# Optimization experiments

Measured on AMD Instinct MI355X. Metric: run time of the kernel, lower is better.

Reference implementation:

```python
import jax, jax.numpy as jnp
import numpy as np

EMBED_DIM = 512
NUM_HEADS = 8
HEAD_DIM = EMBED_DIM // NUM_HEADS
SCALE = 1.0 / HEAD_DIM ** 0.5


def setup_inputs() -> dict:
    key = jax.random.key(0)
    ks = jax.random.split(key, 7)
    B, C, H, W = 8, EMBED_DIM, 32, 32
    x = jax.random.normal(ks[0], (B, C, H, W), dtype=jnp.float32)
    s = 1.0 / np.sqrt(EMBED_DIM)
    return {
        "x": x,
        "ln_gamma": jnp.ones((EMBED_DIM,), jnp.float32),
        "ln_beta": jnp.zeros((EMBED_DIM,), jnp.float32),
        "w_qkv": jax.random.uniform(ks[1], (EMBED_DIM, 3 * EMBED_DIM), jnp.float32, -s, s),
        "b_qkv": jax.random.uniform(ks[2], (3 * EMBED_DIM,), jnp.float32, -s, s),
        "w_proj": jax.random.uniform(ks[3], (EMBED_DIM, EMBED_DIM), jnp.float32, -s, s),
        "b_proj": jax.random.uniform(ks[4], (EMBED_DIM,), jnp.float32, -s, s),
    }


def reference(x, ln_gamma, ln_beta, w_qkv, b_qkv, w_proj, b_proj):
    B, C, H, W = x.shape
    N = H * W
    # LayerNorm over channel dim (applied in NHWC layout in the original)
    xs = x.reshape(B, C, N).transpose(0, 2, 1)  # [B, N, C]
    mu = jnp.mean(xs, axis=-1, keepdims=True)
    var = jnp.mean(jnp.square(xs - mu), axis=-1, keepdims=True)
    xn = (xs - mu) / jnp.sqrt(var + 1e-5) * ln_gamma + ln_beta
    # QKV projection
    qkv = xn @ w_qkv + b_qkv                        # [B, N, 3C]
    qkv = qkv.reshape(B, N, 3, NUM_HEADS, HEAD_DIM)
    q = qkv[:, :, 0].transpose(0, 2, 1, 3)         # [B, h, N, d]
    k = qkv[:, :, 1].transpose(0, 2, 1, 3)
    v = qkv[:, :, 2].transpose(0, 2, 1, 3)
    # Scaled dot-product attention (full N x N scores, as in source)
    attn = jnp.einsum('bhnd,bhmd->bhnm', q, k) * SCALE
    attn = jax.nn.softmax(attn, axis=-1)
    o = jnp.einsum('bhnm,bhmd->bhnd', attn, v)     # [B, h, N, d]
    o = o.transpose(0, 2, 1, 3).reshape(B, N, C)
    # Output projection (dropout is identity in eval)
    o = o @ w_proj + b_proj
    return o.transpose(0, 2, 1).reshape(B, C, H, W)
```

## Files before the change

kernel.cpp:

```cpp
#include <hip/hip_runtime.h>
#include <hip/hip_bf16.h>
#include <math.h>

#define B_   8
#define C_   512
#define NH_  8
#define HD_  64
#define NSP  1024
#define M_   (B_*NSP)
#define NQKV 1536
#define SCALE_ 0.125f
#define S2L_  0.18033688f

typedef __attribute__((ext_vector_type(8))) __bf16 bf16x8;
typedef __attribute__((ext_vector_type(4))) float  f32x4;
typedef __attribute__((ext_vector_type(16))) float f32x16;

__device__ __forceinline__ unsigned short f2bf(float f) {
  unsigned int u = __float_as_uint(f);
  u = u + 0x7fffu + ((u >> 16) & 1u);
  return (unsigned short)(u >> 16);
}

__device__ __forceinline__ unsigned int pk2bf(float a, float b) {
  __hip_bfloat162 t = __float22bfloat162_rn(make_float2(a, b));
  unsigned int u; __builtin_memcpy(&u, &t, 4);
  return u;
}

__device__ __forceinline__ void async16(const unsigned short* g, unsigned short* l) {
  __builtin_amdgcn_global_load_lds(
      (const __attribute__((address_space(1))) void*)g,
      (__attribute__((address_space(3))) void*)l, 16, 0, 0);
}

__global__ void ln_stats_kernel(const float* __restrict__ x,
                                float* __restrict__ psum,
                                float* __restrict__ psum2) {
  int tx = threadIdx.x & 31, ty = threadIdx.x >> 5;
  int cg  = blockIdx.x & 3;
  int nch = (blockIdx.x >> 2) & 31;
  int b   = blockIdx.x >> 7;
  int n0 = nch * 32;
  const float* xp = x + (size_t)b * C_ * NSP + n0 + tx;
  float s = 0.f, s2 = 0.f;
  for (int c = cg * 128 + ty; c < cg * 128 + 128; c += 8) {
    float v = xp[(size_t)c * NSP];
    s += v; s2 += v * v;
  }
  __shared__ float sh_s[8][32], sh_s2[8][32];
  sh_s[ty][tx] = s; sh_s2[ty][tx] = s2;
  __syncthreads();
  if (ty == 0) {
    float S = 0.f, S2 = 0.f;
    for (int j = 0; j < 8; j++) { S += sh_s[j][tx]; S2 += sh_s2[j][tx]; }
    psum [cg * M_ + b * NSP + n0 + tx] = S;
    psum2[cg * M_ + b * NSP + n0 + tx] = S2;
  }
}

__global__ __launch_bounds__(256) void applyw_kernel(
    const float* __restrict__ x, const float* __restrict__ psum,
    const float* __restrict__ psum2, const float* __restrict__ gamma,
    const float* __restrict__ beta, const float* __restrict__ wqkv,
    const float* __restrict__ wproj, unsigned short* __restrict__ xn,
    unsigned short* __restrict__ wqkvT, unsigned short* __restrict__ wprojT) {
  int tid = threadIdx.x;
  __shared__ float tile[64][65];
  int tx = tid & 63, ty = tid >> 6;
  if (blockIdx.x >= 1024) {
    const float* W; unsigned short* WT; int NW, t;
    if (blockIdx.x < 1216) { W = wqkv;  WT = wqkvT;  NW = NQKV; t = blockIdx.x - 1024; }
    else                   { W = wproj; WT = wprojT; NW = C_;   t = blockIdx.x - 1216; }
    int ntiles = NW >> 6;
    int kt = t / ntiles, nt = t - kt * ntiles;
    for (int i = ty; i < 64; i += 4)
      tile[i][tx] = W[(size_t)(kt * 64 + i) * NW + nt * 64 + tx];
    __syncthreads();
    for (int i = ty; i < 64; i += 4)
      WT[(size_t)(nt * 64 + i) * C_ + kt * 64 + tx] = f2bf(tile[tx][i]);
    return;
  }
  __shared__ float smu[64], srs[64];
  int c0 = (blockIdx.x & 7) * 64;
  int n0 = ((blockIdx.x >> 3) & 15) * 64;
  int b  = blockIdx.x >> 7;
  if (tid < 64) {
    int n = b * NSP + n0 + tid;
    float s  = psum [n] + psum [M_ + n] + psum [2 * M_ + n] + psum [3 * M_ + n];
    float s2 = psum2[n] + psum2[M_ + n] + psum2[2 * M_ + n] + psum2[3 * M_ + n];
    float mu = s * (1.0f / C_);
    float var = s2 * (1.0f / C_) - mu * mu;
    smu[tid] = mu;
    srs[tid] = rsqrtf(var + 1e-5f);
  }
  const float* xp = x + ((size_t)b * C_ + c0) * NSP + n0;
  for (int i = ty; i < 64; i += 4)
    tile[i][tx] = xp[(size_t)i * NSP + tx];
  __syncthreads();
  float g = gamma[c0 + tx], be = beta[c0 + tx];
  unsigned short* op = xn + ((size_t)(b * NSP + n0)) * C_ + c0 + tx;
  for (int i = ty; i < 64; i += 4) {
    float v = (tile[tx][i] - smu[i]) * srs[i] * g + be;
    op[(size_t)i * C_] = f2bf(v);
  }
}

__global__ __launch_bounds__(256, 3) void gemm_qkv_kernel(
    const unsigned short* __restrict__ A,
    const unsigned short* __restrict__ Bt,
    const float* __restrict__ bias,
    unsigned short* __restrict__ out0, unsigned short* __restrict__ out1) {
  __shared__ __align__(16) char smem[32768];
  int tid = threadIdx.x;
  int wave = tid >> 6, lane = tid & 63, quad = lane >> 4, l15 = lane & 15;
  int n0 = blockIdx.x * 128, m0 = blockIdx.y * 128;
  int wm = (wave >> 1) * 64, wn = (wave & 1) * 64;
  int srow = lane >> 2, schunk = (lane & 3) * 8;
  auto stage = [&](int k0, int buf) {
    unsigned short* As = (unsigned short*)(smem + buf * 16384);
    unsigned short* Bs = (unsigned short*)(smem + buf * 16384 + 8192);
#pragma unroll
    for (int j = 0; j < 2; j++) {
      int r0 = (wave + 4 * j) * 16;
      async16(A + (size_t)(m0 + r0 + srow) * 512 + k0 + schunk, As + r0 * 32 + lane * 8);
      async16(Bt + (size_t)(n0 + r0 + srow) * 512 + k0 + schunk, Bs + r0 * 32 + lane * 8);
    }
  };
  f32x4 acc[4][4] = {};
  stage(0, 0);
  for (int kt = 0; kt < 16; kt++) {
    int cur = kt & 1;
    __syncthreads();
    if (kt < 15) stage((kt + 1) * 32, cur ^ 1);
    unsigned short* As = (unsigned short*)(smem + cur * 16384);
    unsigned short* Bs = (unsigned short*)(smem + cur * 16384 + 8192);
    bf16x8 a[4], bb[4];
#pragma unroll
    for (int mt = 0; mt < 4; mt++)
      a[mt] = *(const bf16x8*)(As + (wm + mt * 16 + l15) * 32 + quad * 8);
#pragma unroll
    for (int nt = 0; nt < 4; nt++)
      bb[nt] = *(const bf16x8*)(Bs + (wn + nt * 16 + l15) * 32 + quad * 8);
#pragma unroll
    for (int mt = 0; mt < 4; mt++)
#pragma unroll
      for (int nt = 0; nt < 4; nt++)
        acc[mt][nt] = __builtin_amdgcn_mfma_f32_16x16x32_bf16(
            a[mt], bb[nt], acc[mt][nt], 0, 0, 0);
  }
  __syncthreads();
  float bw[4];
#pragma unroll
  for (int nt = 0; nt < 4; nt++) bw[nt] = bias[n0 + wn + nt * 16 + l15];
  if (n0 < 1024) {
    float sc = ((n0 + wn) < 512) ? S2L_ : 1.0f;
    unsigned short* buf = (unsigned short*)(smem + wave * 8192);
#pragma unroll
    for (int p = 0; p < 2; p++) {
#pragma unroll
      for (int mh = 0; mh < 2; mh++) {
        int mt = p * 2 + mh;
#pragma unroll
        for (int nt = 0; nt < 4; nt++)
#pragma unroll
          for (int r = 0; r < 4; r++)
            buf[(mh * 16 + quad * 4 + r) * 68 + nt * 16 + l15] =
                f2bf((acc[mt][nt][r] + bw[nt]) * sc);
      }
#pragma unroll
      for (int i = 0; i < 4; i++) {
        int row = i * 8 + (lane >> 3);
        const unsigned short* bp_ = &buf[row * 68 + (lane & 7) * 8];
        uint2 lo = *(const uint2*)bp_;
        uint2 hi = *(const uint2*)(bp_ + 4);
        *(uint4*)(out0 + (size_t)(m0 + wm + p * 32 + row) * 1024 +
                  n0 + wn + (lane & 7) * 8) = make_uint4(lo.x, lo.y, hi.x, hi.y);
      }
    }
  } else {
    unsigned short* buf = (unsigned short*)(smem + wave * 8192);
    int b = m0 >> 10, nbase = m0 & 1023;
    for (int nc = 0; nc < 4; nc++) {
#pragma unroll
      for (int mt = 0; mt < 4; mt++)
#pragma unroll
        for (int r = 0; r < 4; r++)
          buf[(mt * 16 + quad * 4 + r) * 17 + l15] = f2bf(acc[mt][nc][r] + bw[nc]);
#pragma unroll
      for (int cl = 0; cl < 16; cl++) {
        int crel = n0 - 1024 + wn + nc * 16 + cl;
        out1[((size_t)b * C_ + crel) * NSP + nbase + wm + lane] = buf[lane * 17 + cl];
      }
    }
  }
}

__global__ __launch_bounds__(256) void gemm_proj_kernel(
    const unsigned short* __restrict__ A,
    const unsigned short* __restrict__ Bt,
    const float* __restrict__ bias,
    float* __restrict__ O) {
  __shared__ __align__(16) char smem[24576];
  int tid = threadIdx.x;
  int wave = tid >> 6, lane = tid & 63, quad = lane >> 4, l15 = lane & 15;
  int n0 = blockIdx.x * 128, m0 = blockIdx.y * 64;
  int wm = (wave >> 1) * 32, wn = (wave & 1) * 64;
  int srow = lane >> 2, schunk = (lane & 3) * 8;
  auto stage = [&](int k0, int buf) {
    unsigned short* As = (unsigned short*)(smem + buf * 12288);
    unsigned short* Bs = (unsigned short*)(smem + buf * 12288 + 4096);
    async16(A + (size_t)(m0 + wave * 16 + srow) * 512 + k0 + schunk,
            As + wave * 16 * 32 + lane * 8);
#pragma unroll
    for (int j = 0; j < 2; j++) {
      int r0 = (wave + 4 * j) * 16;
      async16(Bt + (size_t)(n0 + r0 + srow) * 512 + k0 + schunk, Bs + r0 * 32 + lane * 8);
    }
  };
  f32x4 acc[2][4] = {};
  stage(0, 0);
  for (int kt = 0; kt < 16; kt++) {
    int cur = kt & 1;
    __syncthreads();
    if (kt < 15) stage((kt + 1) * 32, cur ^ 1);
    unsigned short* As = (unsigned short*)(smem + cur * 12288);
    unsigned short* Bs = (unsigned short*)(smem + cur * 12288 + 4096);
    bf16x8 a[2], bb[4];
#pragma unroll
    for (int mt = 0; mt < 2; mt++)
      a[mt] = *(const bf16x8*)(As + (wm + mt * 16 + l15) * 32 + quad * 8);
#pragma unroll
    for (int nt = 0; nt < 4; nt++)
      bb[nt] = *(const bf16x8*)(Bs + (wn + nt * 16 + l15) * 32 + quad * 8);
#pragma unroll
    for (int mt = 0; mt < 2; mt++)
#pragma unroll
      for (int nt = 0; nt < 4; nt++)
        acc[mt][nt] = __builtin_amdgcn_mfma_f32_16x16x32_bf16(
            a[mt], bb[nt], acc[mt][nt], 0, 0, 0);
  }
  __syncthreads();
  float bw[4];
#pragma unroll
  for (int nt = 0; nt < 4; nt++) bw[nt] = bias[n0 + wn + nt * 16 + l15];
  float* buf = (float*)(smem + wave * 6144);
  int b = m0 >> 10, nbase = m0 & 1023;
  int ml = lane & 31, cg = lane >> 5;
  for (int nc = 0; nc < 4; nc++) {
#pragma unroll
    for (int mt = 0; mt < 2; mt++)
#pragma unroll
      for (int r = 0; r < 4; r++)
        buf[(mt * 16 + quad * 4 + r) * 17 + l15] = acc[mt][nc][r] + bw[nc];
#pragma unroll
    for (int j = 0; j < 8; j++) {
      int cl = j * 2 + cg;
      int c = n0 + wn + nc * 16 + cl;
      O[((size_t)b * C_ + c) * NSP + nbase + wm + ml] = buf[ml * 17 + cl];
    }
  }
}

__global__ __launch_bounds__(256, 2) void attn_kernel(
    const unsigned short* __restrict__ qk,
    const unsigned short* __restrict__ vt,
    unsigned short* __restrict__ o_ws) {
  __shared__ __align__(16) unsigned short Ks[2][64][64];
  __shared__ __align__(16) unsigned short Vts[2][64][64];
  int tid = threadIdx.x;
  int wave = tid >> 6, lane = tid & 63;
  int l31 = lane & 31, hi = lane >> 5;
  int b = blockIdx.x >> 3, h = blockIdx.x & 7;
  int qb = blockIdx.y * 128 + wave * 32;
  int sc8 = lane & 7, sr8 = lane >> 3;
  int swz = sc8 ^ sr8;
  bf16x8 bq[4];
#pragma unroll
  for (int ks = 0; ks < 4; ks++)
    bq[ks] = *(const bf16x8*)(
        qk + (size_t)(b * NSP + qb + l31) * 1024 + h * 64 + ks * 16 + hi * 8);
  auto stage = [&](int it, int buf) {
    int k0 = it * 64;
#pragma unroll
    for (int g = 0; g < 2; g++) {
      int row = wave * 16 + g * 8 + sr8;
      async16(qk + (size_t)(b * NSP + k0 + row) * 1024 + 512 + h * 64 + swz * 8,
              &Ks[buf][wave * 16 + g * 8][0]);
      async16(vt + ((size_t)(b * C_ + h * 64 + row)) * NSP + k0 + swz * 8,
              &Vts[buf][wave * 16 + g * 8][0]);
    }
  };
  f32x16 ot0 = {}, ot1 = {};
  float lsum = 0.f;
  stage(0, 0);
  for (int it = 0; it < 16; it++) {
    int cur = it & 1;
    __syncthreads();
    if (it < 15) stage(it + 1, cur ^ 1);
    bf16x8 bp[4];
#pragma unroll
    for (int kt = 0; kt < 2; kt++) {
      f32x16 s = {};
#pragma unroll
      for (int ks = 0; ks < 4; ks++) {
        bf16x8 ak = *(const bf16x8*)(
            &Ks[cur][kt * 32 + l31][((ks * 2 + hi) ^ (l31 & 7)) * 8]);
        s = __builtin_amdgcn_mfma_f32_32x32x16_bf16(ak, bq[ks], s, 0, 0, 0);
      }
      float p0 = __builtin_amdgcn_exp2f(s[0]),  p1 = __builtin_amdgcn_exp2f(s[1]);
      float p2 = __builtin_amdgcn_exp2f(s[2]),  p3 = __builtin_amdgcn_exp2f(s[3]);
      float p4 = __builtin_amdgcn_exp2f(s[4]),  p5 = __builtin_amdgcn_exp2f(s[5]);
      float p6 = __builtin_amdgcn_exp2f(s[6]),  p7 = __builtin_amdgcn_exp2f(s[7]);
      float p8 = __builtin_amdgcn_exp2f(s[8]),  p9 = __builtin_amdgcn_exp2f(s[9]);
      float pa = __builtin_amdgcn_exp2f(s[10]), pb = __builtin_amdgcn_exp2f(s[11]);
      float pc = __builtin_amdgcn_exp2f(s[12]), pd = __builtin_amdgcn_exp2f(s[13]);
      float pe = __builtin_amdgcn_exp2f(s[14]), pf = __builtin_amdgcn_exp2f(s[15]);
      lsum += ((p0 + p1) + (p2 + p3)) + ((p4 + p5) + (p6 + p7)) +
              (((p8 + p9) + (pa + pb)) + ((pc + pd) + (pe + pf)));
      unsigned int d0 = pk2bf(p0, p1), d1 = pk2bf(p2, p3);
      unsigned int d2 = pk2bf(p4, p5), d3 = pk2bf(p6, p7);
      unsigned int d4 = pk2bf(p8, p9), d5 = pk2bf(pa, pb);
      unsigned int d6 = pk2bf(pc, pd), d7 = pk2bf(pe, pf);
      asm volatile("v_permlane32_swap_b32 %0, %1" : "+v"(d0), "+v"(d2));
      asm volatile("v_permlane32_swap_b32 %0, %1" : "+v"(d1), "+v"(d3));
      asm volatile("v_permlane32_swap_b32 %0, %1" : "+v"(d4), "+v"(d6));
      asm volatile("v_permlane32_swap_b32 %0, %1" : "+v"(d5), "+v"(d7));
      uint4 f0 = make_uint4(d0, d1, d2, d3);
      uint4 f1 = make_uint4(d4, d5, d6, d7);
      __builtin_memcpy(&bp[kt * 2 + 0], &f0, 16);
      __builtin_memcpy(&bp[kt * 2 + 1], &f1, 16);
    }
#pragma unroll
    for (int kc = 0; kc < 4; kc++) {
      bf16x8 av0 = *(const bf16x8*)(
          &Vts[cur][l31][((kc * 2 + hi) ^ (l31 & 7)) * 8]);
      ot0 = __builtin_amdgcn_mfma_f32_32x32x16_bf16(av0, bp[kc], ot0, 0, 0, 0);
      bf16x8 av1 = *(const bf16x8*)(
          &Vts[cur][32 + l31][(((kc * 2 + hi) ^ (l31 & 7)) ^ 0) * 8]);
      ot1 = __builtin_amdgcn_mfma_f32_32x32x16_bf16(av1, bp[kc], ot1, 0, 0, 0);
    }
  }
  float lv = __shfl(lsum, l31) + __shfl(lsum, l31 + 32);
  float inv = 1.f / lv;
  unsigned short* orow = o_ws + (size_t)(b * NSP + qb + l31) * 512 + h * 64;
#pragma unroll
  for (int g = 0; g < 4; g++) {
    int d0 = 8 * g + 4 * hi;
    *(uint2*)(orow + d0) =
        make_uint2(pk2bf(ot0[4 * g + 0] * inv, ot0[4 * g + 1] * inv),
                   pk2bf(ot0[4 * g + 2] * inv, ot0[4 * g + 3] * inv));
    *(uint2*)(orow + 32 + d0) =
        make_uint2(pk2bf(ot1[4 * g + 0] * inv, ot1[4 * g + 1] * inv),
                   pk2bf(ot1[4 * g + 2] * inv, ot1[4 * g + 3] * inv));
  }
}

extern "C" void kernel_launch(void* const* d_in, const int* in_sizes, int n_in,
                              void* d_out, int out_size, void* d_ws, size_t ws_size,
                              hipStream_t stream) {
  const float* x     = (const float*)d_in[0];
  const float* gamma = (const float*)d_in[1];
  const float* beta  = (const float*)d_in[2];
  const float* wqkv  = (const float*)d_in[3];
  const float* bqkv  = (const float*)d_in[4];
  const float* wproj = (const float*)d_in[5];
  const float* bproj = (const float*)d_in[6];
  char* ws = (char*)d_ws;
  float*          psum   = (float*)ws;
  float*          psum2  = (float*)(ws + 131072);
  unsigned short* wqkvT  = (unsigned short*)(ws + 262144);
  unsigned short* wprojT = (unsigned short*)(ws + 1835008);
  unsigned short* qk_bf  = (unsigned short*)(ws + 2359296);
  unsigned short* vt_bf  = (unsigned short*)(ws + 19136512);
  unsigned short* xn_bf  = (unsigned short*)(ws + 27525120);
  unsigned short* o_bf   = xn_bf;
  float* out = (float*)d_out;

  ln_stats_kernel<<<1024, 256, 0, stream>>>(x, psum, psum2);
  applyw_kernel<<<1024 + 192 + 64, 256, 0, stream>>>(x, psum, psum2, gamma, beta,
                                                     wqkv, wproj, xn_bf, wqkvT, wprojT);
  gemm_qkv_kernel<<<dim3(NQKV / 128, M_ / 128), 256, 0, stream>>>(
      xn_bf, wqkvT, bqkv, qk_bf, vt_bf);
  attn_kernel<<<dim3(B_ * NH_, NSP / 64 / 2), 256, 0, stream>>>(qk_bf, vt_bf, o_bf);
  gemm_proj_kernel<<<dim3(C_ / 128, M_ / 64), 256, 0, stream>>>(
      o_bf, wprojT, bproj, out);
}
```

Baseline: 149.3 us.

## Process two query tiles per wave in attention to reuse K/V fragments

```diff
diff --git a/kernel.cpp b/kernel.cpp
--- a/kernel.cpp
+++ b/kernel.cpp
@@ -262,7 +262,7 @@
   }
 }
 
-__global__ __launch_bounds__(256, 2) void attn_kernel(
+__global__ __launch_bounds__(256, 1) void attn_kernel(
     const unsigned short* __restrict__ qk,
     const unsigned short* __restrict__ vt,
     unsigned short* __restrict__ o_ws) {
@@ -272,14 +272,17 @@
   int wave = tid >> 6, lane = tid & 63;
   int l31 = lane & 31, hi = lane >> 5;
   int b = blockIdx.x >> 3, h = blockIdx.x & 7;
-  int qb = blockIdx.y * 128 + wave * 32;
+  int qb = blockIdx.y * 256 + wave * 64;
   int sc8 = lane & 7, sr8 = lane >> 3;
   int swz = sc8 ^ sr8;
-  bf16x8 bq[4];
-#pragma unroll
-  for (int ks = 0; ks < 4; ks++)
-    bq[ks] = *(const bf16x8*)(
-        qk + (size_t)(b * NSP + qb + l31) * 1024 + h * 64 + ks * 16 + hi * 8);
+  bf16x8 bq[2][4];
+#pragma unroll
+  for (int qs = 0; qs < 2; qs++)
+#pragma unroll
+    for (int ks = 0; ks < 4; ks++)
+      bq[qs][ks] = *(const bf16x8*)(
+          qk + (size_t)(b * NSP + qb + qs * 32 + l31) * 1024 +
+          h * 64 + ks * 16 + hi * 8);
   auto stage = [&](int it, int buf) {
     int k0 = it * 64;
 #pragma unroll
@@ -291,68 +294,79 @@
               &Vts[buf][wave * 16 + g * 8][0]);
     }
   };
-  f32x16 ot0 = {}, ot1 = {};
-  float lsum = 0.f;
+  f32x16 ot[2][2] = {};
+  float lsum[2] = {0.f, 0.f};
   stage(0, 0);
   for (int it = 0; it < 16; it++) {
     int cur = it & 1;
     __syncthreads();
     if (it < 15) stage(it + 1, cur ^ 1);
-    bf16x8 bp[4];
+    bf16x8 bp[2][4];
 #pragma unroll
     for (int kt = 0; kt < 2; kt++) {
-      f32x16 s = {};
-#pragma unroll
-      for (int ks = 0; ks < 4; ks++) {
-        bf16x8 ak = *(const bf16x8*)(
+      bf16x8 ak[4];
+#pragma unroll
+      for (int ks = 0; ks < 4; ks++)
+        ak[ks] = *(const bf16x8*)(
             &Ks[cur][kt * 32 + l31][((ks * 2 + hi) ^ (l31 & 7)) * 8]);
-        s = __builtin_amdgcn_mfma_f32_32x32x16_bf16(ak, bq[ks], s, 0, 0, 0);
+#pragma unroll
+      for (int qs = 0; qs < 2; qs++) {
+        f32x16 s = {};
+#pragma unroll
+        for (int ks = 0; ks < 4; ks++)
+          s = __builtin_amdgcn_mfma_f32_32x32x16_bf16(ak[ks], bq[qs][ks], s, 0, 0, 0);
+        float p0 = __builtin_amdgcn_exp2f(s[0]),  p1 = __builtin_amdgcn_exp2f(s[1]);
+        float p2 = __builtin_amdgcn_exp2f(s[2]),  p3 = __builtin_amdgcn_exp2f(s[3]);
+        float p4 = __builtin_amdgcn_exp2f(s[4]),  p5 = __builtin_amdgcn_exp2f(s[5]);
+        float p6 = __builtin_amdgcn_exp2f(s[6]),  p7 = __builtin_amdgcn_exp2f(s[7]);
+        float p8 = __builtin_amdgcn_exp2f(s[8]),  p9 = __builtin_amdgcn_exp2f(s[9]);
+        float pa = __builtin_amdgcn_exp2f(s[10]), pb = __builtin_amdgcn_exp2f(s[11]);
+        float pc = __builtin_amdgcn_exp2f(s[12]), pd = __builtin_amdgcn_exp2f(s[13]);
+        float pe = __builtin_amdgcn_exp2f(s[14]), pf = __builtin_amdgcn_exp2f(s[15]);
+        lsum[qs] += ((p0 + p1) + (p2 + p3)) + ((p4 + p5) + (p6 + p7)) +
+                    (((p8 + p9) + (pa + pb)) + ((pc + pd) + (pe + pf)));
+        unsigned int d0 = pk2bf(p0, p1), d1 = pk2bf(p2, p3);
+        unsigned int d2 = pk2bf(p4, p5), d3 = pk2bf(p6, p7);
+        unsigned int d4 = pk2bf(p8, p9), d5 = pk2bf(pa, pb);
+        unsigned int d6 = pk2bf(pc, pd), d7 = pk2bf(pe, pf);
+        asm volatile("v_permlane32_swap_b32 %0, %1" : "+v"(d0), "+v"(d2));
+        asm volatile("v_permlane32_swap_b32 %0, %1" : "+v"(d1), "+v"(d3));
+        asm volatile("v_permlane32_swap_b32 %0, %1" : "+v"(d4), "+v"(d6));
+        asm volatile("v_permlane32_swap_b32 %0, %1" : "+v"(d5), "+v"(d7));
+        uint4 f0 = make_uint4(d0, d1, d2, d3);
+        uint4 f1 = make_uint4(d4, d5, d6, d7);
+        __builtin_memcpy(&bp[qs][kt * 2 + 0], &f0, 16);
+        __builtin_memcpy(&bp[qs][kt * 2 + 1], &f1, 16);
       }
-      float p0 = __builtin_amdgcn_exp2f(s[0]),  p1 = __builtin_amdgcn_exp2f(s[1]);
-      float p2 = __builtin_amdgcn_exp2f(s[2]),  p3 = __builtin_amdgcn_exp2f(s[3]);
-      float p4 = __builtin_amdgcn_exp2f(s[4]),  p5 = __builtin_amdgcn_exp2f(s[5]);
-      float p6 = __builtin_amdgcn_exp2f(s[6]),  p7 = __builtin_amdgcn_exp2f(s[7]);
-      float p8 = __builtin_amdgcn_exp2f(s[8]),  p9 = __builtin_amdgcn_exp2f(s[9]);
-      float pa = __builtin_amdgcn_exp2f(s[10]), pb = __builtin_amdgcn_exp2f(s[11]);
-      float pc = __builtin_amdgcn_exp2f(s[12]), pd = __builtin_amdgcn_exp2f(s[13]);
-      float pe = __builtin_amdgcn_exp2f(s[14]), pf = __builtin_amdgcn_exp2f(s[15]);
-      lsum += ((p0 + p1) + (p2 + p3)) + ((p4 + p5) + (p6 + p7)) +
-              (((p8 + p9) + (pa + pb)) + ((pc + pd) + (pe + pf)));
-      unsigned int d0 = pk2bf(p0, p1), d1 = pk2bf(p2, p3);
-      unsigned int d2 = pk2bf(p4, p5), d3 = pk2bf(p6, p7);
-      unsigned int d4 = pk2bf(p8, p9), d5 = pk2bf(pa, pb);
-      unsigned int d6 = pk2bf(pc, pd), d7 = pk2bf(pe, pf);
-      asm volatile("v_permlane32_swap_b32 %0, %1" : "+v"(d0), "+v"(d2));
-      asm volatile("v_permlane32_swap_b32 %0, %1" : "+v"(d1), "+v"(d3));
-      asm volatile("v_permlane32_swap_b32 %0, %1" : "+v"(d4), "+v"(d6));
-      asm volatile("v_permlane32_swap_b32 %0, %1" : "+v"(d5), "+v"(d7));
-      uint4 f0 = make_uint4(d0, d1, d2, d3);
-      uint4 f1 = make_uint4(d4, d5, d6, d7);
-      __builtin_memcpy(&bp[kt * 2 + 0], &f0, 16);
-      __builtin_memcpy(&bp[kt * 2 + 1], &f1, 16);
     }
 #pragma unroll
     for (int kc = 0; kc < 4; kc++) {
       bf16x8 av0 = *(const bf16x8*)(
           &Vts[cur][l31][((kc * 2 + hi) ^ (l31 & 7)) * 8]);
-      ot0 = __builtin_amdgcn_mfma_f32_32x32x16_bf16(av0, bp[kc], ot0, 0, 0, 0);
       bf16x8 av1 = *(const bf16x8*)(
-          &Vts[cur][32 + l31][(((kc * 2 + hi) ^ (l31 & 7)) ^ 0) * 8]);
-      ot1 = __builtin_amdgcn_mfma_f32_32x32x16_bf16(av1, bp[kc], ot1, 0, 0, 0);
-    }
-  }
-  float lv = __shfl(lsum, l31) + __shfl(lsum, l31 + 32);
-  float inv = 1.f / lv;
-  unsigned short* orow = o_ws + (size_t)(b * NSP + qb + l31) * 512 + h * 64;
-#pragma unroll
-  for (int g = 0; g < 4; g++) {
-    int d0 = 8 * g + 4 * hi;
-    *(uint2*)(orow + d0) =
-        make_uint2(pk2bf(ot0[4 * g + 0] * inv, ot0[4 * g + 1] * inv),
-                   pk2bf(ot0[4 * g + 2] * inv, ot0[4 * g + 3] * inv));
-    *(uint2*)(orow + 32 + d0) =
-        make_uint2(pk2bf(ot1[4 * g + 0] * inv, ot1[4 * g + 1] * inv),
-                   pk2bf(ot1[4 * g + 2] * inv, ot1[4 * g + 3] * inv));
+          &Vts[cur][32 + l31][((kc * 2 + hi) ^ (l31 & 7)) * 8]);
+#pragma unroll
+      for (int qs = 0; qs < 2; qs++) {
+        ot[qs][0] = __builtin_amdgcn_mfma_f32_32x32x16_bf16(av0, bp[qs][kc], ot[qs][0], 0, 0, 0);
+        ot[qs][1] = __builtin_amdgcn_mfma_f32_32x32x16_bf16(av1, bp[qs][kc], ot[qs][1], 0, 0, 0);
+      }
+    }
+  }
+#pragma unroll
+  for (int qs = 0; qs < 2; qs++) {
+    float lv = __shfl(lsum[qs], l31) + __shfl(lsum[qs], l31 + 32);
+    float inv = 1.f / lv;
+    unsigned short* orow = o_ws + (size_t)(b * NSP + qb + qs * 32 + l31) * 512 + h * 64;
+#pragma unroll
+    for (int g = 0; g < 4; g++) {
+      int d0 = 8 * g + 4 * hi;
+      *(uint2*)(orow + d0) =
+          make_uint2(pk2bf(ot[qs][0][4 * g + 0] * inv, ot[qs][0][4 * g + 1] * inv),
+                     pk2bf(ot[qs][0][4 * g + 2] * inv, ot[qs][0][4 * g + 3] * inv));
+      *(uint2*)(orow + 32 + d0) =
+          make_uint2(pk2bf(ot[qs][1][4 * g + 0] * inv, ot[qs][1][4 * g + 1] * inv),
+                     pk2bf(ot[qs][1][4 * g + 2] * inv, ot[qs][1][4 * g + 3] * inv));
+    }
   }
 }
 
@@ -382,7 +396,7 @@
                                                      wqkv, wproj, xn_bf, wqkvT, wprojT);
   gemm_qkv_kernel<<<dim3(NQKV / 128, M_ / 128), 256, 0, stream>>>(
       xn_bf, wqkvT, bqkv, qk_bf, vt_bf);
-  attn_kernel<<<dim3(B_ * NH_, NSP / 64 / 2), 256, 0, stream>>>(qk_bf, vt_bf, o_bf);
+  attn_kernel<<<dim3(B_ * NH_, NSP / 256), 256, 0, stream>>>(qk_bf, vt_bf, o_bf);
   gemm_proj_kernel<<<dim3(C_ / 128, M_ / 64), 256, 0, stream>>>(
       o_bf, wprojT, bproj, out);
 }
```

Measured after the change: 159.5 us. +6.8%, slower.

## Fuse LayerNorm stats into apply kernel and split attention keys across waves

Applied to the files above, without the earlier changes.

```diff
diff --git a/kernel.cpp b/kernel.cpp
--- a/kernel.cpp
+++ b/kernel.cpp
@@ -34,44 +34,20 @@
       (__attribute__((address_space(3))) void*)l, 16, 0, 0);
 }
 
-__global__ void ln_stats_kernel(const float* __restrict__ x,
-                                float* __restrict__ psum,
-                                float* __restrict__ psum2) {
-  int tx = threadIdx.x & 31, ty = threadIdx.x >> 5;
-  int cg  = blockIdx.x & 3;
-  int nch = (blockIdx.x >> 2) & 31;
-  int b   = blockIdx.x >> 7;
-  int n0 = nch * 32;
-  const float* xp = x + (size_t)b * C_ * NSP + n0 + tx;
-  float s = 0.f, s2 = 0.f;
-  for (int c = cg * 128 + ty; c < cg * 128 + 128; c += 8) {
-    float v = xp[(size_t)c * NSP];
-    s += v; s2 += v * v;
-  }
-  __shared__ float sh_s[8][32], sh_s2[8][32];
-  sh_s[ty][tx] = s; sh_s2[ty][tx] = s2;
-  __syncthreads();
-  if (ty == 0) {
-    float S = 0.f, S2 = 0.f;
-    for (int j = 0; j < 8; j++) { S += sh_s[j][tx]; S2 += sh_s2[j][tx]; }
-    psum [cg * M_ + b * NSP + n0 + tx] = S;
-    psum2[cg * M_ + b * NSP + n0 + tx] = S2;
-  }
-}
-
-__global__ __launch_bounds__(256) void applyw_kernel(
-    const float* __restrict__ x, const float* __restrict__ psum,
-    const float* __restrict__ psum2, const float* __restrict__ gamma,
+__global__ __launch_bounds__(256) void ln_fused_kernel(
+    const float* __restrict__ x, const float* __restrict__ gamma,
     const float* __restrict__ beta, const float* __restrict__ wqkv,
     const float* __restrict__ wproj, unsigned short* __restrict__ xn,
     unsigned short* __restrict__ wqkvT, unsigned short* __restrict__ wprojT) {
+  __shared__ __align__(16) char smem[76032];
+  __shared__ float smu[32], srs[32];
   int tid = threadIdx.x;
-  __shared__ float tile[64][65];
-  int tx = tid & 63, ty = tid >> 6;
-  if (blockIdx.x >= 1024) {
+  if (blockIdx.x >= 256) {
+    float (*tile)[65] = (float(*)[65])smem;
+    int tx = tid & 63, ty = tid >> 6;
     const float* W; unsigned short* WT; int NW, t;
-    if (blockIdx.x < 1216) { W = wqkv;  WT = wqkvT;  NW = NQKV; t = blockIdx.x - 1024; }
-    else                   { W = wproj; WT = wprojT; NW = C_;   t = blockIdx.x - 1216; }
+    if (blockIdx.x < 448) { W = wqkv;  WT = wqkvT;  NW = NQKV; t = blockIdx.x - 256; }
+    else                  { W = wproj; WT = wprojT; NW = C_;   t = blockIdx.x - 448; }
     int ntiles = NW >> 6;
     int kt = t / ntiles, nt = t - kt * ntiles;
     for (int i = ty; i < 64; i += 4)
@@ -81,28 +57,44 @@
       WT[(size_t)(nt * 64 + i) * C_ + kt * 64 + tx] = f2bf(tile[tx][i]);
     return;
   }
-  __shared__ float smu[64], srs[64];
-  int c0 = (blockIdx.x & 7) * 64;
-  int n0 = ((blockIdx.x >> 3) & 15) * 64;
-  int b  = blockIdx.x >> 7;
-  if (tid < 64) {
-    int n = b * NSP + n0 + tid;
-    float s  = psum [n] + psum [M_ + n] + psum [2 * M_ + n] + psum [3 * M_ + n];
-    float s2 = psum2[n] + psum2[M_ + n] + psum2[2 * M_ + n] + psum2[3 * M_ + n];
-    float mu = s * (1.0f / C_);
-    float var = s2 * (1.0f / C_) - mu * mu;
+  float (*tile)[33] = (float(*)[33])smem;
+  float (*shs)[33]  = (float(*)[33])(smem + 67584);
+  float (*shs2)[33] = (float(*)[33])(smem + 67584 + 4224);
+  int b = blockIdx.x >> 5, n0 = (blockIdx.x & 31) * 32;
+  int tx8 = tid & 7, cy = tid >> 3;
+  float s[4] = {}, q[4] = {};
+  const float* xp = x + ((size_t)b * C_) * NSP + n0 + tx8 * 4;
+#pragma unroll
+  for (int i = 0; i < 16; i++) {
+    int c = cy + i * 32;
+    float4 v = *(const float4*)(xp + (size_t)c * NSP);
+    tile[c][tx8 * 4 + 0] = v.x; tile[c][tx8 * 4 + 1] = v.y;
+    tile[c][tx8 * 4 + 2] = v.z; tile[c][tx8 * 4 + 3] = v.w;
+    s[0] += v.x; q[0] += v.x * v.x;  s[1] += v.y; q[1] += v.y * v.y;
+    s[2] += v.z; q[2] += v.z * v.z;  s[3] += v.w; q[3] += v.w * v.w;
+  }
+#pragma unroll
+  for (int j = 0; j < 4; j++) { shs[cy][tx8 * 4 + j] = s[j]; shs2[cy][tx8 * 4 + j] = q[j]; }
+  __syncthreads();
+  if (tid < 32) {
+    float S = 0.f, S2 = 0.f;
+#pragma unroll
+    for (int r = 0; r < 32; r++) { S += shs[r][tid]; S2 += shs2[r][tid]; }
+    float mu = S * (1.0f / C_);
+    float var = S2 * (1.0f / C_) - mu * mu;
     smu[tid] = mu;
     srs[tid] = rsqrtf(var + 1e-5f);
   }
-  const float* xp = x + ((size_t)b * C_ + c0) * NSP + n0;
-  for (int i = ty; i < 64; i += 4)
-    tile[i][tx] = xp[(size_t)i * NSP + tx];
-  __syncthreads();
-  float g = gamma[c0 + tx], be = beta[c0 + tx];
-  unsigned short* op = xn + ((size_t)(b * NSP + n0)) * C_ + c0 + tx;
-  for (int i = ty; i < 64; i += 4) {
-    float v = (tile[tx][i] - smu[i]) * srs[i] * g + be;
-    op[(size_t)i * C_] = f2bf(v);
+  __syncthreads();
+  int c2 = tid * 2;
+  float g0 = gamma[c2], g1 = gamma[c2 + 1], be0 = beta[c2], be1 = beta[c2 + 1];
+  unsigned short* op = xn + ((size_t)(b * NSP + n0)) * C_ + c2;
+#pragma unroll
+  for (int n = 0; n < 32; n++) {
+    float mu = smu[n], rs = srs[n];
+    float v0 = (tile[c2][n]     - mu) * rs * g0 + be0;
+    float v1 = (tile[c2 + 1][n] - mu) * rs * g1 + be1;
+    *(unsigned int*)(op + (size_t)n * C_) = pk2bf(v0, v1);
   }
 }
 
@@ -262,17 +254,18 @@
   }
 }
 
-__global__ __launch_bounds__(256, 2) void attn_kernel(
+__global__ __launch_bounds__(256, 4) void attn_kernel(
     const unsigned short* __restrict__ qk,
     const unsigned short* __restrict__ vt,
     unsigned short* __restrict__ o_ws) {
-  __shared__ __align__(16) unsigned short Ks[2][64][64];
-  __shared__ __align__(16) unsigned short Vts[2][64][64];
+  __shared__ __align__(16) unsigned short Ks[2][2][32][64];
+  __shared__ __align__(16) unsigned short Vts[2][2][4][64][8];
   int tid = threadIdx.x;
   int wave = tid >> 6, lane = tid & 63;
   int l31 = lane & 31, hi = lane >> 5;
+  int qw = wave & 1, kh = wave >> 1;
   int b = blockIdx.x >> 3, h = blockIdx.x & 7;
-  int qb = blockIdx.y * 128 + wave * 32;
+  int qb = blockIdx.y * 64 + qw * 32;
   int sc8 = lane & 7, sr8 = lane >> 3;
   int swz = sc8 ^ sr8;
   bf16x8 bq[4];
@@ -281,78 +274,94 @@
     bq[ks] = *(const bf16x8*)(
         qk + (size_t)(b * NSP + qb + l31) * 1024 + h * 64 + ks * 16 + hi * 8);
   auto stage = [&](int it, int buf) {
-    int k0 = it * 64;
-#pragma unroll
-    for (int g = 0; g < 2; g++) {
-      int row = wave * 16 + g * 8 + sr8;
-      async16(qk + (size_t)(b * NSP + k0 + row) * 1024 + 512 + h * 64 + swz * 8,
-              &Ks[buf][wave * 16 + g * 8][0]);
-      async16(vt + ((size_t)(b * C_ + h * 64 + row)) * NSP + k0 + swz * 8,
-              &Vts[buf][wave * 16 + g * 8][0]);
+    int k0 = kh * 512 + it * 32;
+#pragma unroll
+    for (int j = 0; j < 2; j++) {
+      int row = qw * 16 + j * 8;
+      async16(qk + (size_t)(b * NSP + k0 + row + sr8) * 1024 + 512 + h * 64 + swz * 8,
+              &Ks[buf][kh][row][0]);
+      int ch = qw * 2 + j;
+      async16(vt + ((size_t)(b * C_ + h * 64 + lane)) * NSP + k0 + ch * 8,
+              &Vts[buf][kh][ch][0][0]);
     }
   };
-  f32x16 ot0 = {}, ot1 = {};
+  f32x16 ot[2] = {};
   float lsum = 0.f;
   stage(0, 0);
   for (int it = 0; it < 16; it++) {
     int cur = it & 1;
     __syncthreads();
     if (it < 15) stage(it + 1, cur ^ 1);
-    bf16x8 bp[4];
-#pragma unroll
-    for (int kt = 0; kt < 2; kt++) {
-      f32x16 s = {};
-#pragma unroll
-      for (int ks = 0; ks < 4; ks++) {
-        bf16x8 ak = *(const bf16x8*)(
-            &Ks[cur][kt * 32 + l31][((ks * 2 + hi) ^ (l31 & 7)) * 8]);
-        s = __builtin_amdgcn_mfma_f32_32x32x16_bf16(ak, bq[ks], s, 0, 0, 0);
-      }
-      float p0 = __builtin_amdgcn_exp2f(s[0]),  p1 = __builtin_amdgcn_exp2f(s[1]);
-      float p2 = __builtin_amdgcn_exp2f(s[2]),  p3 = __builtin_amdgcn_exp2f(s[3]);
-      float p4 = __builtin_amdgcn_exp2f(s[4]),  p5 = __builtin_amdgcn_exp2f(s[5]);
-      float p6 = __builtin_amdgcn_exp2f(s[6]),  p7 = __builtin_amdgcn_exp2f(s[7]);
-      float p8 = __builtin_amdgcn_exp2f(s[8]),  p9 = __builtin_amdgcn_exp2f(s[9]);
-      float pa = __builtin_amdgcn_exp2f(s[10]), pb = __builtin_amdgcn_exp2f(s[11]);
-      float pc = __builtin_amdgcn_exp2f(s[12]), pd = __builtin_amdgcn_exp2f(s[13]);
-      float pe = __builtin_amdgcn_exp2f(s[14]), pf = __builtin_amdgcn_exp2f(s[15]);
-      lsum += ((p0 + p1) + (p2 + p3)) + ((p4 + p5) + (p6 + p7)) +
-              (((p8 + p9) + (pa + pb)) + ((pc + pd) + (pe + pf)));
-      unsigned int d0 = pk2bf(p0, p1), d1 = pk2bf(p2, p3);
-      unsigned int d2 = pk2bf(p4, p5), d3 = pk2bf(p6, p7);
-      unsigned int d4 = pk2bf(p8, p9), d5 = pk2bf(pa, pb);
-      unsigned int d6 = pk2bf(pc, pd), d7 = pk2bf(pe, pf);
-      asm volatile("v_permlane32_swap_b32 %0, %1" : "+v"(d0), "+v"(d2));
-      asm volatile("v_permlane32_swap_b32 %0, %1" : "+v"(d1), "+v"(d3));
-      asm volatile("v_permlane32_swap_b32 %0, %1" : "+v"(d4), "+v"(d6));
-      asm volatile("v_permlane32_swap_b32 %0, %1" : "+v"(d5), "+v"(d7));
-      uint4 f0 = make_uint4(d0, d1, d2, d3);
-      uint4 f1 = make_uint4(d4, d5, d6, d7);
-      __builtin_memcpy(&bp[kt * 2 + 0], &f0, 16);
-      __builtin_memcpy(&bp[kt * 2 + 1], &f1, 16);
-    }
-#pragma unroll
-    for (int kc = 0; kc < 4; kc++) {
-      bf16x8 av0 = *(const bf16x8*)(
-          &Vts[cur][l31][((kc * 2 + hi) ^ (l31 & 7)) * 8]);
-      ot0 = __builtin_amdgcn_mfma_f32_32x32x16_bf16(av0, bp[kc], ot0, 0, 0, 0);
-      bf16x8 av1 = *(const bf16x8*)(
-          &Vts[cur][32 + l31][(((kc * 2 + hi) ^ (l31 & 7)) ^ 0) * 8]);
-      ot1 = __builtin_amdgcn_mfma_f32_32x32x16_bf16(av1, bp[kc], ot1, 0, 0, 0);
-    }
-  }
-  float lv = __shfl(lsum, l31) + __shfl(lsum, l31 + 32);
-  float inv = 1.f / lv;
-  unsigned short* orow = o_ws + (size_t)(b * NSP + qb + l31) * 512 + h * 64;
-#pragma unroll
-  for (int g = 0; g < 4; g++) {
-    int d0 = 8 * g + 4 * hi;
-    *(uint2*)(orow + d0) =
-        make_uint2(pk2bf(ot0[4 * g + 0] * inv, ot0[4 * g + 1] * inv),
-                   pk2bf(ot0[4 * g + 2] * inv, ot0[4 * g + 3] * inv));
-    *(uint2*)(orow + 32 + d0) =
-        make_uint2(pk2bf(ot1[4 * g + 0] * inv, ot1[4 * g + 1] * inv),
-                   pk2bf(ot1[4 * g + 2] * inv, ot1[4 * g + 3] * inv));
+    f32x16 s = {};
+#pragma unroll
+    for (int ks = 0; ks < 4; ks++) {
+      bf16x8 ak = *(const bf16x8*)(
+          &Ks[cur][kh][l31][((ks * 2 + hi) ^ (l31 & 7)) * 8]);
+      s = __builtin_amdgcn_mfma_f32_32x32x16_bf16(ak, bq[ks], s, 0, 0, 0);
+    }
+    float p0 = __builtin_amdgcn_exp2f(s[0]),  p1 = __builtin_amdgcn_exp2f(s[1]);
+    float p2 = __builtin_amdgcn_exp2f(s[2]),  p3 = __builtin_amdgcn_exp2f(s[3]);
+    float p4 = __builtin_amdgcn_exp2f(s[4]),  p5 = __builtin_amdgcn_exp2f(s[5]);
+    float p6 = __builtin_amdgcn_exp2f(s[6]),  p7 = __builtin_amdgcn_exp2f(s[7]);
+    float p8 = __builtin_amdgcn_exp2f(s[8]),  p9 = __builtin_amdgcn_exp2f(s[9]);
+    float pa = __builtin_amdgcn_exp2f(s[10]), pb = __builtin_amdgcn_exp2f(s[11]);
+    float pc = __builtin_amdgcn_exp2f(s[12]), pd = __builtin_amdgcn_exp2f(s[13]);
+    float pe = __builtin_amdgcn_exp2f(s[14]), pf = __builtin_amdgcn_exp2f(s[15]);
+    lsum += ((p0 + p1) + (p2 + p3)) + ((p4 + p5) + (p6 + p7)) +
+            (((p8 + p9) + (pa + pb)) + ((pc + pd) + (pe + pf)));
+    unsigned int d0 = pk2bf(p0, p1), d1 = pk2bf(p2, p3);
+    unsigned int d2 = pk2bf(p4, p5), d3 = pk2bf(p6, p7);
+    unsigned int d4 = pk2bf(p8, p9), d5 = pk2bf(pa, pb);
+    unsigned int d6 = pk2bf(pc, pd), d7 = pk2bf(pe, pf);
+    asm volatile("v_permlane32_swap_b32 %0, %1" : "+v"(d0), "+v"(d2));
+    asm volatile("v_permlane32_swap_b32 %0, %1" : "+v"(d1), "+v"(d3));
+    asm volatile("v_permlane32_swap_b32 %0, %1" : "+v"(d4), "+v"(d6));
+    asm volatile("v_permlane32_swap_b32 %0, %1" : "+v"(d5), "+v"(d7));
+    bf16x8 bp[2];
+    uint4 f0 = make_uint4(d0, d1, d2, d3);
+    uint4 f1 = make_uint4(d4, d5, d6, d7);
+    __builtin_memcpy(&bp[0], &f0, 16);
+    __builtin_memcpy(&bp[1], &f1, 16);
+#pragma unroll
+    for (int kc = 0; kc < 2; kc++) {
+      bf16x8 av0 = *(const bf16x8*)(&Vts[cur][kh][kc * 2 + hi][l31][0]);
+      bf16x8 av1 = *(const bf16x8*)(&Vts[cur][kh][kc * 2 + hi][32 + l31][0]);
+      ot[0] = __builtin_amdgcn_mfma_f32_32x32x16_bf16(av0, bp[kc], ot[0], 0, 0, 0);
+      ot[1] = __builtin_amdgcn_mfma_f32_32x32x16_bf16(av1, bp[kc], ot[1], 0, 0, 0);
+    }
+  }
+  __syncthreads();
+  float* Cb = (float*)&Ks[0][0][0][0];
+  float* Lb = (float*)&Vts[0][0][0][0][0];
+  if (kh == 1) {
+#pragma unroll
+    for (int dh = 0; dh < 2; dh++)
+#pragma unroll
+      for (int e = 0; e < 16; e++)
+        Cb[((qw * 2 + dh) * 16 + e) * 64 + lane] = ot[dh][e];
+    Lb[qw * 64 + lane] = lsum;
+  }
+  __syncthreads();
+  if (kh == 0) {
+#pragma unroll
+    for (int dh = 0; dh < 2; dh++)
+#pragma unroll
+      for (int e = 0; e < 16; e++)
+        ot[dh][e] += Cb[((qw * 2 + dh) * 16 + e) * 64 + lane];
+    float lo = lsum + Lb[qw * 64 + lane];
+    float lv = __shfl(lo, l31) + __shfl(lo, l31 + 32);
+    float inv = 1.f / lv;
+    unsigned short* orow = o_ws + (size_t)(b * NSP + qb + l31) * 512 + h * 64;
+#pragma unroll
+    for (int g = 0; g < 4; g++) {
+      int d0 = 8 * g + 4 * hi;
+      *(uint2*)(orow + d0) =
+          make_uint2(pk2bf(ot[0][4 * g + 0] * inv, ot[0][4 * g + 1] * inv),
+                     pk2bf(ot[0][4 * g + 2] * inv, ot[0][4 * g + 3] * inv));
+      *(uint2*)(orow + 32 + d0) =
+          make_uint2(pk2bf(ot[1][4 * g + 0] * inv, ot[1][4 * g + 1] * inv),
+                     pk2bf(ot[1][4 * g + 2] * inv, ot[1][4 * g + 3] * inv));
+    }
   }
 }
 
@@ -367,8 +376,6 @@
   const float* wproj = (const float*)d_in[5];
   const float* bproj = (const float*)d_in[6];
   char* ws = (char*)d_ws;
-  float*          psum   = (float*)ws;
-  float*          psum2  = (float*)(ws + 131072);
   unsigned short* wqkvT  = (unsigned short*)(ws + 262144);
   unsigned short* wprojT = (unsigned short*)(ws + 1835008);
   unsigned short* qk_bf  = (unsigned short*)(ws + 2359296);
@@ -377,12 +384,11 @@
   unsigned short* o_bf   = xn_bf;
   float* out = (float*)d_out;
 
-  ln_stats_kernel<<<1024, 256, 0, stream>>>(x, psum, psum2);
-  applyw_kernel<<<1024 + 192 + 64, 256, 0, stream>>>(x, psum, psum2, gamma, beta,
-                                                     wqkv, wproj, xn_bf, wqkvT, wprojT);
+  ln_fused_kernel<<<256 + 192 + 64, 256, 0, stream>>>(
+      x, gamma, beta, wqkv, wproj, xn_bf, wqkvT, wprojT);
   gemm_qkv_kernel<<<dim3(NQKV / 128, M_ / 128), 256, 0, stream>>>(
       xn_bf, wqkvT, bqkv, qk_bf, vt_bf);
-  attn_kernel<<<dim3(B_ * NH_, NSP / 64 / 2), 256, 0, stream>>>(qk_bf, vt_bf, o_bf);
+  attn_kernel<<<dim3(B_ * NH_, NSP / 64), 256, 0, stream>>>(qk_bf, vt_bf, o_bf);
   gemm_proj_kernel<<<dim3(C_ / 128, M_ / 64), 256, 0, stream>>>(
       o_bf, wprojT, bproj, out);
 }
```

Measured after the change: 147.9 us. About the same (-1.0%).
